# Optimization experiments

Measured on AMD Instinct MI355X. Metric: run time of the kernel, lower is better.

Reference implementation:

```python
import jax, jax.numpy as jnp
import numpy as np
from jax import lax

COCO_80_TO_91 = [1,2,3,4,5,6,7,8,9,10,11,13,14,15,16,17,18,19,20,21,22,23,24,25,27,28,31,32,33,34,35,36,37,38,39,40,41,42,43,44,46,47,48,49,50,51,52,53,54,55,56,57,58,59,60,61,62,63,64,65,67,70,72,73,74,75,76,77,78,79,80,81,82,84,85,86,87,88,89,90]

CONF = 0.25      # self.confidence
IOU_THR = 0.7    # ultralytics NMS default
TOPK = 1000      # candidate cap before NMS
MAX_DET = 300    # ultralytics max_det default
MAX_WH = 7680.0  # per-class offset trick
IMG_SZ = 640.0   # yolov8 letterboxed input size


def setup_inputs() -> dict:
    key = jax.random.key(0)
    preds = jax.random.uniform(key, (32, 84, 8400), dtype=jnp.float32)
    return {"preds": preds}


def _nms_single(boxes, scores):
    """Greedy NMS on score-descending boxes [K,4] (class-offset xyxy). Returns keep mask [K]."""
    K = boxes.shape[0]
    area = (boxes[:, 2] - boxes[:, 0]) * (boxes[:, 3] - boxes[:, 1])  # [K]
    lt = jnp.maximum(boxes[:, None, :2], boxes[None, :, :2])          # [K,K,2]
    rb = jnp.minimum(boxes[:, None, 2:], boxes[None, :, 2:])
    wh = jnp.clip(rb - lt, 0.0)
    inter = wh[..., 0] * wh[..., 1]
    iou = inter / (area[:, None] + area[None, :] - inter + 1e-7)       # [K,K]
    idx = jnp.arange(K)
    sup = (iou > IOU_THR) & (idx[None, :] > idx[:, None])              # i suppresses later j

    def body(i, keep):
        return jnp.where(keep[i], keep & ~sup[i], keep)

    return lax.fori_loop(0, K, body, jnp.ones((K,), dtype=bool))


def reference(preds):
    # preds: [B, 84, N] -> [B, N, 84]
    p = jnp.transpose(preds, (0, 2, 1))
    box_xywh = p[..., :4] * IMG_SZ           # xywh in pixels on 640x640 canvas
    cls = p[..., 4:]                          # [B, N, 80]
    scores = jnp.max(cls, axis=-1)            # best-class confidence
    labels = jnp.argmax(cls, axis=-1)         # 0..79
    xy, wh = box_xywh[..., :2], box_xywh[..., 2:]
    xyxy = jnp.concatenate([xy - wh * 0.5, xy + wh * 0.5], axis=-1)  # decode

    # confidence filter + top-K candidate selection (score-descending)
    s_masked = jnp.where(scores > CONF, scores, -1.0)
    top_s, top_i = lax.top_k(s_masked, TOPK)                          # [B,TOPK]
    top_b = jnp.take_along_axis(xyxy, top_i[..., None], axis=1)      # [B,TOPK,4]
    top_l = jnp.take_along_axis(labels, top_i, axis=1)               # [B,TOPK]

    # per-class NMS via class offset
    off_b = top_b + (top_l.astype(top_b.dtype) * MAX_WH)[..., None]
    keep = jax.vmap(_nms_single)(off_b, top_s) & (top_s > CONF)

    # select final max_det detections, zero-pad invalid slots
    fin_s = jnp.where(keep, top_s, -1.0)
    out_s, out_i = lax.top_k(fin_s, MAX_DET)                          # [B,MAX_DET]
    out_b = jnp.take_along_axis(top_b, out_i[..., None], axis=1)
    out_l = jnp.take_along_axis(top_l, out_i, axis=1)
    valid = out_s > CONF
    boxes = jnp.where(valid[..., None], out_b, 0.0)
    scores_out = jnp.where(valid, out_s, 0.0)
    mapped = jnp.asarray(COCO_80_TO_91, dtype=jnp.int64)[out_l]       # COCO 80 -> 91 ids
    labels_out = jnp.where(valid, mapped, 0)
    return boxes, scores_out, labels_out
```

## Files before the change

kernel.cpp:

```cpp
#include <hip/hip_runtime.h>
#include <stdint.h>

typedef unsigned long long u64;
typedef unsigned int u32;

#define BATCH 32
#define NCH 84
#define NA 8400
#define NCLS 80
#define TOPK 1000
#define MAXDET 300
#define CONF 0.25f
#define IOU_T 0.7f
#define MAX_WH 7680.0f
#define IMG_SZ 640.0f
#define NT 1024
#define KPT 9
#define NCOPY 8
#define HPAD 260
#define DTILE 256

__device__ __constant__ float coco_map_f[NCLS] = {
    1,2,3,4,5,6,7,8,9,10,11,13,14,15,16,17,18,19,20,21,22,23,24,25,27,28,
    31,32,33,34,35,36,37,38,39,40,41,42,43,44,46,47,48,49,50,51,52,53,54,
    55,56,57,58,59,60,61,62,63,64,65,67,70,72,73,74,75,76,77,78,79,80,81,
    82,84,85,86,87,88,89,90};

__device__ inline u64 shflx64(u64 v, int m) {
    int lo = __shfl_xor((int)(u32)(v & 0xFFFFFFFFull), m, 64);
    int hi = __shfl_xor((int)(u32)(v >> 32), m, 64);
    return ((u64)(u32)hi << 32) | (u32)lo;
}

__global__ __launch_bounds__(256)
void decode_kernel(const float* __restrict__ preds,
                   u64* __restrict__ keys,
                   float4* __restrict__ boxes,
                   int* __restrict__ labels) {
    const int b = blockIdx.y;
    const int a_base = blockIdx.x * DTILE;
    const int t = threadIdx.x;
    const int a = a_base + t;
    const float* p = preds + (size_t)b * NCH * NA;

    __shared__ float stage[16][DTILE];

    float bx = 0.f, by = 0.f, bw = 0.f, bh = 0.f;
    float best = -1.0f;
    int bl = 0;

    for (int chunk = 0; chunk < 6; ++chunk) {
        const int r0 = chunk * 16;
        const int nr = (chunk == 5) ? 4 : 16;
        if (chunk) __syncthreads();
        for (int i = 0; i < nr / 4; ++i) {
            int idx = i * 256 + t;
            int rl = idx >> 6;
            int c4 = (idx & 63) * 4;
            int col = a_base + c4;
            float4 v = (col < NA) ? *(const float4*)(p + (size_t)(r0 + rl) * NA + col)
                                  : make_float4(0.f, 0.f, 0.f, 0.f);
            *(float4*)&stage[rl][c4] = v;
        }
        __syncthreads();
        if (chunk == 0) {
            bx = stage[0][t]; by = stage[1][t];
            bw = stage[2][t]; bh = stage[3][t];
            best = stage[4][t]; bl = 0;
            for (int r = 5; r < 16; ++r) {
                float v = stage[r][t];
                int c = r - 4;
                bl = (v > best) ? c : bl;  best = fmaxf(v, best);
            }
        } else {
            for (int r = 0; r < nr; ++r) {
                float v = stage[r][t];
                int c = r0 + r - 4;
                bl = (v > best) ? c : bl;  best = fmaxf(v, best);
            }
        }
    }

    if (a < NA) {
        float fx = bx * IMG_SZ, fy = by * IMG_SZ;
        float fw = bw * IMG_SZ, fh = bh * IMG_SZ;
        float hw = fw * 0.5f, hh = fh * 0.5f;
        boxes[(size_t)b * NA + a] = make_float4(fx - hw, fy - hh, fx + hw, fy + hh);
        float s = (best > CONF) ? best : -1.0f;
        u32 fb = __float_as_uint(s);
        u32 u = (fb & 0x80000000u) ? ~fb : (fb | 0x80000000u);
        keys[(size_t)b * NA + a] = ((u64)u << 14) | (u64)(16383 - a);
        labels[(size_t)b * NA + a] = bl;
    }
}

__global__ __launch_bounds__(NT)
void select_sort_kernel(const u64* __restrict__ keys,
                        const float4* __restrict__ boxes,
                        const int* __restrict__ labels,
                        u64* __restrict__ sortedk,
                        float4* __restrict__ gbox,
                        float4* __restrict__ goffr,
                        float* __restrict__ garear,
                        unsigned char* __restrict__ lbr,
                        float4* __restrict__ goffb,
                        float* __restrict__ garea,
                        unsigned short* __restrict__ grank,
                        int* __restrict__ gccnt) {
    const int b = blockIdx.x;
    const int t = threadIdx.x;
    const int lane = t & 63, wid = t >> 6;

    __shared__ union {
        struct {
            u64 sk[2][NT];
            int hist[NCOPY * HPAD];
        } a;
        struct {
            u64 cmask2[NCLS][16];
        } bb;
    } u_s;
    __shared__ int selB, selK, hselS, smax, scnt, cnt;

    u64 kreg[KPT];
    const u64* kb = keys + (size_t)b * NA;
    int nk = 0;
    for (int i = t; i < NA; i += NT) kreg[nk++] = kb[i];

    u64 P = 0ull;
    int kk = TOPK;
    int nsel = 0;
    for (int d = 5; d >= 0; --d) {
        __syncthreads();
        if (t == 0) { smax = -1; scnt = 0; }
        __syncthreads();
        u64 hmask = (~0ull) << (8 * (d + 1));
        int dig[KPT];
        int mymax = -1;
#pragma unroll
        for (int i = 0; i < KPT; ++i) {
            bool act = (i < nk) && (((kreg[i] ^ P) & hmask) == 0ull);
            dig[i] = act ? (int)((kreg[i] >> (8 * d)) & 255) : -1;
            mymax = max(mymax, dig[i]);
        }
#pragma unroll
        for (int off = 32; off; off >>= 1)
            mymax = max(mymax, __shfl_down(mymax, off, 64));
        if (lane == 0) atomicMax(&smax, mymax);
        __syncthreads();
        int maxb = smax;
        int myc = 0;
#pragma unroll
        for (int i = 0; i < KPT; ++i) myc += (dig[i] == maxb) ? 1 : 0;
#pragma unroll
        for (int off = 32; off; off >>= 1) myc += __shfl_down(myc, off, 64);
        if (lane == 0) atomicAdd(&scnt, myc);
        __syncthreads();
        int cm = scnt;
        if (cm >= kk) {
            P |= ((u64)maxb) << (8 * d);
            nsel = TOPK - kk + cm;
            if (nsel <= NT) break;
            continue;
        }
        for (int i = t; i < NCOPY * HPAD; i += NT) u_s.a.hist[i] = 0;
        __syncthreads();
        int* myh = u_s.a.hist + (wid & (NCOPY - 1)) * HPAD;
#pragma unroll
        for (int i = 0; i < KPT; ++i)
            if (dig[i] >= 0) atomicAdd(&myh[dig[i]], 1);
        __syncthreads();
        if (t < 64) {
            int h0 = 0, h1 = 0, h2 = 0, h3 = 0;
            for (int c = 0; c < NCOPY; ++c) {
                const int* hp = u_s.a.hist + c * HPAD + 4 * t;
                h0 += hp[0]; h1 += hp[1]; h2 += hp[2]; h3 += hp[3];
            }
            int s = h0 + h1 + h2 + h3;
            int S = s;
            #pragma unroll
            for (int off = 1; off < 64; off <<= 1) {
                int o = __shfl_down(S, off, 64);
                if (t + off < 64) S += o;
            }
            int Snext = S - s;
            int c3 = Snext + h3, c2 = c3 + h2, c1 = c2 + h1, c0 = c1 + h0;
            int cand = -1, above = 0;
            if (c0 >= kk) {
                if      (c3 >= kk) { cand = 4 * t + 3; above = Snext; }
                else if (c2 >= kk) { cand = 4 * t + 2; above = c3; }
                else if (c1 >= kk) { cand = 4 * t + 1; above = c2; }
                else               { cand = 4 * t;     above = c1; }
            }
            int pc = (cand < 0) ? 0 : (((cand + 1) << 16) | (kk - above));
            #pragma unroll
            for (int off = 32; off; off >>= 1)
                pc = max(pc, __shfl_down(pc, off, 64));
            pc = __shfl(pc, 0, 64);
            int B = (pc >> 16) - 1;
            if (t == (B >> 2)) {
                int m4 = B & 3;
                selB = B;
                selK = pc & 0xFFFF;
                hselS = (m4 == 0) ? h0 : (m4 == 1) ? h1 : (m4 == 2) ? h2 : h3;
            }
        }
        __syncthreads();
        P |= ((u64)selB) << (8 * d);
        kk = selK;
        nsel = TOPK - kk + hselS;
        if (nsel <= NT) break;
    }

    __syncthreads();
    if (t == 0) cnt = 0;
    __syncthreads();
    for (int i = 0; i < KPT; ++i) {
        bool p = (i < nk) && (kreg[i] >= P);
        u64 m = __ballot(p);
        int base = 0;
        if (lane == 0) base = atomicAdd(&cnt, (int)__popcll(m));
        base = __shfl(base, 0, 64);
        if (p) u_s.a.sk[0][base + (int)__popcll(m & ((1ull << lane) - 1ull))] = kreg[i];
    }
    if (t < NT - nsel) u_s.a.sk[0][nsel + t] = 0ull;
    __syncthreads();

    u64 myk = u_s.a.sk[0][t];
    int buf = 1;
    for (int size = 2; size <= NT; size <<= 1) {
        bool up = ((t & size) == 0);
        for (int stride = size >> 1; stride; stride >>= 1) {
            u64 pk;
            if (stride >= 64) {
                u_s.a.sk[buf][t] = myk;
                __syncthreads();
                pk = u_s.a.sk[buf][t ^ stride];
                buf ^= 1;
            } else {
                pk = shflx64(myk, stride);
            }
            bool tlow = ((t & stride) == 0);
            u64 mn = (myk < pk) ? myk : pk;
            u64 mx = (myk < pk) ? pk : myk;
            myk = up ? (tlow ? mx : mn) : (tlow ? mn : mx);
        }
    }
    sortedk[(size_t)b * NT + t] = myk;

    __syncthreads();
    for (int i = t; i < NCLS * 16; i += NT) ((u64*)u_s.bb.cmask2)[i] = 0ull;
    __syncthreads();

    int my_L = 0;
    float4 bx = make_float4(0.f, 0.f, 0.f, 0.f);
    float ox0 = 0.f, oy0 = 0.f, ox1 = 0.f, oy1 = 0.f, ar = 0.f;
    if (t < TOPK) {
        int my_a = 16383 - (int)(myk & 16383ull);
        my_L = labels[(size_t)b * NA + my_a];
        bx = boxes[(size_t)b * NA + my_a];
        float off = (float)my_L * MAX_WH;
        ox0 = bx.x + off; oy0 = bx.y + off; ox1 = bx.z + off; oy1 = bx.w + off;
        ar = (ox1 - ox0) * (oy1 - oy0);
        atomicOr(&u_s.bb.cmask2[my_L][t >> 6], 1ull << (t & 63));
    }
    __syncthreads();
    if (t < TOPK) {
        int w = t >> 6;
        int r = __popcll(u_s.bb.cmask2[my_L][w] & ((1ull << (t & 63)) - 1ull));
        for (int q = 0; q < w; ++q) r += __popcll(u_s.bb.cmask2[my_L][q]);
        gbox[(size_t)b * NT + t] = bx;
        goffr[(size_t)b * NT + t] = make_float4(ox0, oy0, ox1, oy1);
        garear[(size_t)b * NT + t] = ar;
        lbr[(size_t)b * NT + t] = (unsigned char)my_L;
        if (r < 64) {
            size_t ci = ((size_t)b * NCLS + my_L) * 64 + r;
            goffb[ci] = make_float4(ox0, oy0, ox1, oy1);
            garea[ci] = ar;
            grank[ci] = (unsigned short)t;
        }
    }
    if (t < NCLS) {
        int s = 0;
#pragma unroll
        for (int q = 0; q < 16; ++q) s += __popcll(u_s.bb.cmask2[t][q]);
        gccnt[(size_t)b * NCLS + t] = s;
    }
}

__global__ __launch_bounds__(64)
void nms_kernel(const float4* __restrict__ goffb,
                const float* __restrict__ garea,
                const unsigned short* __restrict__ grank,
                const int* __restrict__ gccnt,
                const float4* __restrict__ goffr,
                const float* __restrict__ garear,
                const unsigned char* __restrict__ lbr,
                unsigned char* __restrict__ keepg) {
    const int c = blockIdx.x;
    const int b = blockIdx.y;
    const int lane = threadIdx.x;
    const int n = gccnt[(size_t)b * NCLS + c];
    if (n == 0) return;

    if (n <= 64) {
        size_t ci = ((size_t)b * NCLS + c) * 64 + lane;
        float4 bb = make_float4(0.f, 0.f, 0.f, 0.f);
        float ar = 0.f;
        int rk = 0;
        if (lane < n) { bb = goffb[ci]; ar = garea[ci]; rk = grank[ci]; }
        u64 colm = 0ull;
        for (int i = 0; i < n; ++i) {
            float hx0 = __shfl(bb.x, i, 64);
            float hy0 = __shfl(bb.y, i, 64);
            float hx1 = __shfl(bb.z, i, 64);
            float hy1 = __shfl(bb.w, i, 64);
            float ha  = __shfl(ar, i, 64);
            float lx = fmaxf(hx0, bb.x), ly = fmaxf(hy0, bb.y);
            float rx = fminf(hx1, bb.z), ry = fminf(hy1, bb.w);
            float w = fmaxf(rx - lx, 0.0f);
            float h = fmaxf(ry - ly, 0.0f);
            float inter = w * h;
            float denom = ha + ar;
            denom = denom - inter;
            denom = denom + 1e-7f;
            bool s = (lane > i) && (lane < n) && (inter / denom > IOU_T);
            colm |= ((u64)s) << i;
        }
        u64 alive = (n >= 64) ? ~0ull : ((1ull << n) - 1ull);
        for (int i = 0; i < n; ++i) {
            if (!((alive >> i) & 1ull)) continue;
            alive &= ~__ballot((colm >> i) & 1ull);
        }
        if (lane < n) keepg[(size_t)b * NT + rk] = (unsigned char)((alive >> lane) & 1ull);
    } else if (lane == 0) {
        u64 aliveW[16];
        for (int q = 0; q < 16; ++q) aliveW[q] = ~0ull;
        for (int i = 0; i < TOPK; ++i) {
            if (lbr[(size_t)b * NT + i] != (unsigned char)c) continue;
            if (!((aliveW[i >> 6] >> (i & 63)) & 1ull)) continue;
            float4 bi = goffr[(size_t)b * NT + i];
            float ai = garear[(size_t)b * NT + i];
            for (int j = i + 1; j < TOPK; ++j) {
                if (lbr[(size_t)b * NT + j] != (unsigned char)c) continue;
                if (!((aliveW[j >> 6] >> (j & 63)) & 1ull)) continue;
                float4 bj = goffr[(size_t)b * NT + j];
                float lx = fmaxf(bi.x, bj.x), ly = fmaxf(bi.y, bj.y);
                float rx = fminf(bi.z, bj.z), ry = fminf(bi.w, bj.w);
                float w = fmaxf(rx - lx, 0.0f);
                float h = fmaxf(ry - ly, 0.0f);
                float inter = w * h;
                float denom = ai + garear[(size_t)b * NT + j];
                denom = denom - inter;
                denom = denom + 1e-7f;
                if (inter / denom > IOU_T) aliveW[j >> 6] &= ~(1ull << (j & 63));
            }
        }
        for (int i = 0; i < TOPK; ++i)
            if (lbr[(size_t)b * NT + i] == (unsigned char)c)
                keepg[(size_t)b * NT + i] = (unsigned char)((aliveW[i >> 6] >> (i & 63)) & 1ull);
    }
}

__global__ __launch_bounds__(NT)
void epilogue_kernel(const u64* __restrict__ sortedk,
                     const unsigned char* __restrict__ keepg,
                     const float4* __restrict__ gbox,
                     const unsigned char* __restrict__ lbr,
                     float* __restrict__ out) {
    const int b = blockIdx.x;
    const int t = threadIdx.x;
    const int lane = t & 63, wid = t >> 6;
    __shared__ int wsum[16], woff[16], ktot_s;

    u64 myk = sortedk[(size_t)b * NT + t];
    bool valid = false;
    float sj = 0.0f;
    if (t < TOPK) {
        u32 u = (u32)(myk >> 14);
        u32 fb = (u & 0x80000000u) ? (u ^ 0x80000000u) : ~u;
        sj = __uint_as_float(fb);
        valid = keepg[(size_t)b * NT + t] && (sj > CONF);
    }
    u64 m = __ballot(valid);
    if (lane == 0) wsum[wid] = (int)__popcll(m);
    __syncthreads();
    if (wid == 0) {
        int v = (lane < 16) ? wsum[lane] : 0;
        #pragma unroll
        for (int off = 1; off < 16; off <<= 1) {
            int o = __shfl_up(v, off, 64);
            if (lane >= off) v += o;
        }
        if (lane < 16) woff[lane] = v - wsum[lane];
        if (lane == 15) ktot_s = v;
    }
    __syncthreads();
    int ktot = ktot_s;
    int rank = woff[wid] + (int)__popcll(m & ((1ull << lane) - 1ull));

    float* out_boxes = out;
    float* out_scores = out + (size_t)BATCH * MAXDET * 4;
    float* out_labels = out + (size_t)BATCH * MAXDET * 5;
    if (valid && rank < MAXDET) {
        float4 bx = gbox[(size_t)b * NT + t];
        float* ob = out_boxes + ((size_t)b * MAXDET + rank) * 4;
        ob[0] = bx.x; ob[1] = bx.y; ob[2] = bx.z; ob[3] = bx.w;
        out_scores[(size_t)b * MAXDET + rank] = sj;
        out_labels[(size_t)b * MAXDET + rank] = coco_map_f[lbr[(size_t)b * NT + t]];
    }
    if (t < MAXDET && t >= ktot) {
        float* ob = out_boxes + ((size_t)b * MAXDET + t) * 4;
        ob[0] = 0.0f; ob[1] = 0.0f; ob[2] = 0.0f; ob[3] = 0.0f;
        out_scores[(size_t)b * MAXDET + t] = 0.0f;
        out_labels[(size_t)b * MAXDET + t] = 0.0f;
    }
}

extern "C" void kernel_launch(void* const* d_in, const int* in_sizes, int n_in,
                              void* d_out, int out_size, void* d_ws, size_t ws_size,
                              hipStream_t stream) {
    const float* preds = (const float*)d_in[0];
    char* ws = (char*)d_ws;
    size_t off = 0;
    auto alloc = [&](size_t bytes) { char* p = ws + off; off += (bytes + 255) & ~(size_t)255; return p; };

    u64* keys            = (u64*)           alloc((size_t)BATCH * NA * 8);
    float4* boxes        = (float4*)        alloc((size_t)BATCH * NA * 16);
    int* labels          = (int*)           alloc((size_t)BATCH * NA * 4);
    u64* sortedk         = (u64*)           alloc((size_t)BATCH * NT * 8);
    float4* gbox         = (float4*)        alloc((size_t)BATCH * NT * 16);
    float4* goffr        = (float4*)        alloc((size_t)BATCH * NT * 16);
    float* garear        = (float*)         alloc((size_t)BATCH * NT * 4);
    unsigned char* lbr   = (unsigned char*) alloc((size_t)BATCH * NT);
    float4* goffb        = (float4*)        alloc((size_t)BATCH * NCLS * 64 * 16);
    float* garea         = (float*)         alloc((size_t)BATCH * NCLS * 64 * 4);
    unsigned short* grank= (unsigned short*)alloc((size_t)BATCH * NCLS * 64 * 2);
    int* gccnt           = (int*)           alloc((size_t)BATCH * NCLS * 4);
    unsigned char* keepg = (unsigned char*) alloc((size_t)BATCH * NT);
    float* out = (float*)d_out;

    dim3 dgrid((NA + DTILE - 1) / DTILE, BATCH);
    decode_kernel<<<dgrid, 256, 0, stream>>>(preds, keys, boxes, labels);
    select_sort_kernel<<<BATCH, NT, 0, stream>>>(keys, boxes, labels, sortedk,
                                                 gbox, goffr, garear, lbr,
                                                 goffb, garea, grank, gccnt);
    dim3 ngrid(NCLS, BATCH);
    nms_kernel<<<ngrid, 64, 0, stream>>>(goffb, garea, grank, gccnt,
                                         goffr, garear, lbr, keepg);
    epilogue_kernel<<<BATCH, NT, 0, stream>>>(sortedk, keepg, gbox, lbr, out);
}
```

Baseline: 172.5 us.

## Fuse select, NMS and epilogue into one kernel; pack labels into sort keys

```diff
diff --git a/kernel.cpp b/kernel.cpp
--- a/kernel.cpp
+++ b/kernel.cpp
@@ -35,8 +35,7 @@
 __global__ __launch_bounds__(256)
 void decode_kernel(const float* __restrict__ preds,
                    u64* __restrict__ keys,
-                   float4* __restrict__ boxes,
-                   int* __restrict__ labels) {
+                   float4* __restrict__ boxes) {
     const int b = blockIdx.y;
     const int a_base = blockIdx.x * DTILE;
     const int t = threadIdx.x;
@@ -89,24 +88,15 @@
         float s = (best > CONF) ? best : -1.0f;
         u32 fb = __float_as_uint(s);
         u32 u = (fb & 0x80000000u) ? ~fb : (fb | 0x80000000u);
-        keys[(size_t)b * NA + a] = ((u64)u << 14) | (u64)(16383 - a);
-        labels[(size_t)b * NA + a] = bl;
+        keys[(size_t)b * NA + a] =
+            ((u64)u << 21) | ((u64)(16383 - a) << 7) | (u64)bl;
     }
 }
 
 __global__ __launch_bounds__(NT)
-void select_sort_kernel(const u64* __restrict__ keys,
-                        const float4* __restrict__ boxes,
-                        const int* __restrict__ labels,
-                        u64* __restrict__ sortedk,
-                        float4* __restrict__ gbox,
-                        float4* __restrict__ goffr,
-                        float* __restrict__ garear,
-                        unsigned char* __restrict__ lbr,
-                        float4* __restrict__ goffb,
-                        float* __restrict__ garea,
-                        unsigned short* __restrict__ grank,
-                        int* __restrict__ gccnt) {
+void fused_kernel(const u64* __restrict__ keys,
+                  const float4* __restrict__ boxes,
+                  float* __restrict__ out) {
     const int b = blockIdx.x;
     const int t = threadIdx.x;
     const int lane = t & 63, wid = t >> 6;
@@ -119,8 +109,17 @@
         struct {
             u64 cmask2[NCLS][16];
         } bb;
+        struct {
+            float4 obox[NT];
+            float  area[NT];
+            unsigned short ranks[NCLS][64];
+            int    cnt[NCLS];
+            unsigned char cls[NT];
+            unsigned char keep[NT];
+        } c;
     } u_s;
-    __shared__ int selB, selK, hselS, smax, scnt, cnt;
+    __shared__ int selB, selK, hselS, smax, scnt, cnt_s;
+    __shared__ int wsum[16], woff[16], ktot_s;
 
     u64 kreg[KPT];
     const u64* kb = keys + (size_t)b * NA;
@@ -130,7 +129,7 @@
     u64 P = 0ull;
     int kk = TOPK;
     int nsel = 0;
-    for (int d = 5; d >= 0; --d) {
+    for (int d = 6; d >= 0; --d) {
         __syncthreads();
         if (t == 0) { smax = -1; scnt = 0; }
         __syncthreads();
@@ -213,13 +212,13 @@
     }
 
     __syncthreads();
-    if (t == 0) cnt = 0;
+    if (t == 0) cnt_s = 0;
     __syncthreads();
     for (int i = 0; i < KPT; ++i) {
         bool p = (i < nk) && (kreg[i] >= P);
         u64 m = __ballot(p);
         int base = 0;
-        if (lane == 0) base = atomicAdd(&cnt, (int)__popcll(m));
+        if (lane == 0) base = atomicAdd(&cnt_s, (int)__popcll(m));
         base = __shfl(base, 0, 64);
         if (p) u_s.a.sk[0][base + (int)__popcll(m & ((1ull << lane) - 1ull))] = kreg[i];
     }
@@ -246,151 +245,127 @@
             myk = up ? (tlow ? mx : mn) : (tlow ? mn : mx);
         }
     }
-    sortedk[(size_t)b * NT + t] = myk;
 
     __syncthreads();
     for (int i = t; i < NCLS * 16; i += NT) ((u64*)u_s.bb.cmask2)[i] = 0ull;
     __syncthreads();
 
     int my_L = 0;
+    float sj = -1.0f;
     float4 bx = make_float4(0.f, 0.f, 0.f, 0.f);
-    float ox0 = 0.f, oy0 = 0.f, ox1 = 0.f, oy1 = 0.f, ar = 0.f;
     if (t < TOPK) {
-        int my_a = 16383 - (int)(myk & 16383ull);
-        my_L = labels[(size_t)b * NA + my_a];
+        int my_a = 16383 - (int)((myk >> 7) & 16383ull);
+        my_L = (int)(myk & 127ull);
         bx = boxes[(size_t)b * NA + my_a];
-        float off = (float)my_L * MAX_WH;
-        ox0 = bx.x + off; oy0 = bx.y + off; ox1 = bx.z + off; oy1 = bx.w + off;
-        ar = (ox1 - ox0) * (oy1 - oy0);
+        u32 u = (u32)(myk >> 21);
+        u32 fb = (u & 0x80000000u) ? (u ^ 0x80000000u) : ~u;
+        sj = __uint_as_float(fb);
         atomicOr(&u_s.bb.cmask2[my_L][t >> 6], 1ull << (t & 63));
     }
     __syncthreads();
+    int r = 0, cntreg = 0;
     if (t < TOPK) {
         int w = t >> 6;
-        int r = __popcll(u_s.bb.cmask2[my_L][w] & ((1ull << (t & 63)) - 1ull));
+        r = __popcll(u_s.bb.cmask2[my_L][w] & ((1ull << (t & 63)) - 1ull));
         for (int q = 0; q < w; ++q) r += __popcll(u_s.bb.cmask2[my_L][q]);
-        gbox[(size_t)b * NT + t] = bx;
-        goffr[(size_t)b * NT + t] = make_float4(ox0, oy0, ox1, oy1);
-        garear[(size_t)b * NT + t] = ar;
-        lbr[(size_t)b * NT + t] = (unsigned char)my_L;
-        if (r < 64) {
-            size_t ci = ((size_t)b * NCLS + my_L) * 64 + r;
-            goffb[ci] = make_float4(ox0, oy0, ox1, oy1);
-            garea[ci] = ar;
-            grank[ci] = (unsigned short)t;
-        }
     }
     if (t < NCLS) {
-        int s = 0;
-#pragma unroll
-        for (int q = 0; q < 16; ++q) s += __popcll(u_s.bb.cmask2[t][q]);
-        gccnt[(size_t)b * NCLS + t] = s;
-    }
-}
-
-__global__ __launch_bounds__(64)
-void nms_kernel(const float4* __restrict__ goffb,
-                const float* __restrict__ garea,
-                const unsigned short* __restrict__ grank,
-                const int* __restrict__ gccnt,
-                const float4* __restrict__ goffr,
-                const float* __restrict__ garear,
-                const unsigned char* __restrict__ lbr,
-                unsigned char* __restrict__ keepg) {
-    const int c = blockIdx.x;
-    const int b = blockIdx.y;
-    const int lane = threadIdx.x;
-    const int n = gccnt[(size_t)b * NCLS + c];
-    if (n == 0) return;
-
-    if (n <= 64) {
-        size_t ci = ((size_t)b * NCLS + c) * 64 + lane;
-        float4 bb = make_float4(0.f, 0.f, 0.f, 0.f);
-        float ar = 0.f;
-        int rk = 0;
-        if (lane < n) { bb = goffb[ci]; ar = garea[ci]; rk = grank[ci]; }
-        u64 colm = 0ull;
-        for (int i = 0; i < n; ++i) {
-            float hx0 = __shfl(bb.x, i, 64);
-            float hy0 = __shfl(bb.y, i, 64);
-            float hx1 = __shfl(bb.z, i, 64);
-            float hy1 = __shfl(bb.w, i, 64);
-            float ha  = __shfl(ar, i, 64);
-            float lx = fmaxf(hx0, bb.x), ly = fmaxf(hy0, bb.y);
-            float rx = fminf(hx1, bb.z), ry = fminf(hy1, bb.w);
-            float w = fmaxf(rx - lx, 0.0f);
-            float h = fmaxf(ry - ly, 0.0f);
-            float inter = w * h;
-            float denom = ha + ar;
-            denom = denom - inter;
-            denom = denom + 1e-7f;
-            bool s = (lane > i) && (lane < n) && (inter / denom > IOU_T);
-            colm |= ((u64)s) << i;
-        }
-        u64 alive = (n >= 64) ? ~0ull : ((1ull << n) - 1ull);
-        for (int i = 0; i < n; ++i) {
-            if (!((alive >> i) & 1ull)) continue;
-            alive &= ~__ballot((colm >> i) & 1ull);
-        }
-        if (lane < n) keepg[(size_t)b * NT + rk] = (unsigned char)((alive >> lane) & 1ull);
-    } else if (lane == 0) {
-        u64 aliveW[16];
-        for (int q = 0; q < 16; ++q) aliveW[q] = ~0ull;
-        for (int i = 0; i < TOPK; ++i) {
-            if (lbr[(size_t)b * NT + i] != (unsigned char)c) continue;
-            if (!((aliveW[i >> 6] >> (i & 63)) & 1ull)) continue;
-            float4 bi = goffr[(size_t)b * NT + i];
-            float ai = garear[(size_t)b * NT + i];
-            for (int j = i + 1; j < TOPK; ++j) {
-                if (lbr[(size_t)b * NT + j] != (unsigned char)c) continue;
-                if (!((aliveW[j >> 6] >> (j & 63)) & 1ull)) continue;
-                float4 bj = goffr[(size_t)b * NT + j];
-                float lx = fmaxf(bi.x, bj.x), ly = fmaxf(bi.y, bj.y);
-                float rx = fminf(bi.z, bj.z), ry = fminf(bi.w, bj.w);
+#pragma unroll
+        for (int q = 0; q < 16; ++q) cntreg += __popcll(u_s.bb.cmask2[t][q]);
+    }
+    __syncthreads();
+
+    float off = (float)my_L * MAX_WH;
+    float ox0 = bx.x + off, oy0 = bx.y + off, ox1 = bx.z + off, oy1 = bx.w + off;
+    float ar = (ox1 - ox0) * (oy1 - oy0);
+    if (t < TOPK) {
+        u_s.c.obox[t] = make_float4(ox0, oy0, ox1, oy1);
+        u_s.c.area[t] = ar;
+        u_s.c.cls[t]  = (unsigned char)my_L;
+        if (r < 64) u_s.c.ranks[my_L][r] = (unsigned short)t;
+    } else {
+        u_s.c.cls[t] = 255;
+    }
+    u_s.c.keep[t] = 0;
+    if (t < NCLS) u_s.c.cnt[t] = cntreg;
+    __syncthreads();
+
+    for (int cc = wid; cc < NCLS; cc += 16) {
+        int n = u_s.c.cnt[cc];
+        if (n == 0) continue;
+        if (n <= 64) {
+            float4 bbx = make_float4(0.f, 0.f, 0.f, 0.f);
+            float aa = 0.f;
+            int rk = 0;
+            if (lane < n) {
+                rk  = u_s.c.ranks[cc][lane];
+                bbx = u_s.c.obox[rk];
+                aa  = u_s.c.area[rk];
+            }
+            u64 colm = 0ull;
+            for (int i = 0; i < n; ++i) {
+                float hx0 = __shfl(bbx.x, i, 64);
+                float hy0 = __shfl(bbx.y, i, 64);
+                float hx1 = __shfl(bbx.z, i, 64);
+                float hy1 = __shfl(bbx.w, i, 64);
+                float ha  = __shfl(aa, i, 64);
+                float lx = fmaxf(hx0, bbx.x), ly = fmaxf(hy0, bbx.y);
+                float rx = fminf(hx1, bbx.z), ry = fminf(hy1, bbx.w);
                 float w = fmaxf(rx - lx, 0.0f);
                 float h = fmaxf(ry - ly, 0.0f);
                 float inter = w * h;
-                float denom = ai + garear[(size_t)b * NT + j];
+                float denom = ha + aa;
                 denom = denom - inter;
                 denom = denom + 1e-7f;
-                if (inter / denom > IOU_T) aliveW[j >> 6] &= ~(1ull << (j & 63));
-            }
-        }
-        for (int i = 0; i < TOPK; ++i)
-            if (lbr[(size_t)b * NT + i] == (unsigned char)c)
-                keepg[(size_t)b * NT + i] = (unsigned char)((aliveW[i >> 6] >> (i & 63)) & 1ull);
-    }
-}
-
-__global__ __launch_bounds__(NT)
-void epilogue_kernel(const u64* __restrict__ sortedk,
-                     const unsigned char* __restrict__ keepg,
-                     const float4* __restrict__ gbox,
-                     const unsigned char* __restrict__ lbr,
-                     float* __restrict__ out) {
-    const int b = blockIdx.x;
-    const int t = threadIdx.x;
-    const int lane = t & 63, wid = t >> 6;
-    __shared__ int wsum[16], woff[16], ktot_s;
-
-    u64 myk = sortedk[(size_t)b * NT + t];
-    bool valid = false;
-    float sj = 0.0f;
-    if (t < TOPK) {
-        u32 u = (u32)(myk >> 14);
-        u32 fb = (u & 0x80000000u) ? (u ^ 0x80000000u) : ~u;
-        sj = __uint_as_float(fb);
-        valid = keepg[(size_t)b * NT + t] && (sj > CONF);
-    }
+                bool s = (lane > i) && (lane < n) && (inter / denom > IOU_T);
+                colm |= ((u64)s) << i;
+            }
+            u64 alive = (n >= 64) ? ~0ull : ((1ull << n) - 1ull);
+            for (int i = 0; i < n; ++i) {
+                if (!((alive >> i) & 1ull)) continue;
+                alive &= ~__ballot((colm >> i) & 1ull);
+            }
+            if (lane < n) u_s.c.keep[rk] = (unsigned char)((alive >> lane) & 1ull);
+        } else if (lane == 0) {
+            u64 aliveW[16];
+            for (int q = 0; q < 16; ++q) aliveW[q] = ~0ull;
+            for (int i = 0; i < TOPK; ++i) {
+                if (u_s.c.cls[i] != (unsigned char)cc) continue;
+                if (!((aliveW[i >> 6] >> (i & 63)) & 1ull)) continue;
+                float4 bi = u_s.c.obox[i];
+                float ai = u_s.c.area[i];
+                for (int j = i + 1; j < TOPK; ++j) {
+                    if (u_s.c.cls[j] != (unsigned char)cc) continue;
+                    if (!((aliveW[j >> 6] >> (j & 63)) & 1ull)) continue;
+                    float4 bj = u_s.c.obox[j];
+                    float lx = fmaxf(bi.x, bj.x), ly = fmaxf(bi.y, bj.y);
+                    float rx = fminf(bi.z, bj.z), ry = fminf(bi.w, bj.w);
+                    float w = fmaxf(rx - lx, 0.0f);
+                    float h = fmaxf(ry - ly, 0.0f);
+                    float inter = w * h;
+                    float denom = ai + u_s.c.area[j];
+                    denom = denom - inter;
+                    denom = denom + 1e-7f;
+                    if (inter / denom > IOU_T) aliveW[j >> 6] &= ~(1ull << (j & 63));
+                }
+            }
+            for (int i = 0; i < TOPK; ++i)
+                if (u_s.c.cls[i] == (unsigned char)cc)
+                    u_s.c.keep[i] = (unsigned char)((aliveW[i >> 6] >> (i & 63)) & 1ull);
+        }
+    }
+    __syncthreads();
+
+    bool valid = (t < TOPK) && u_s.c.keep[t] && (sj > CONF);
     u64 m = __ballot(valid);
     if (lane == 0) wsum[wid] = (int)__popcll(m);
     __syncthreads();
     if (wid == 0) {
         int v = (lane < 16) ? wsum[lane] : 0;
         #pragma unroll
-        for (int off = 1; off < 16; off <<= 1) {
-            int o = __shfl_up(v, off, 64);
-            if (lane >= off) v += o;
+        for (int o = 1; o < 16; o <<= 1) {
+            int x = __shfl_up(v, o, 64);
+            if (lane >= o) v += x;
         }
         if (lane < 16) woff[lane] = v - wsum[lane];
         if (lane == 15) ktot_s = v;
@@ -403,11 +378,10 @@
     float* out_scores = out + (size_t)BATCH * MAXDET * 4;
     float* out_labels = out + (size_t)BATCH * MAXDET * 5;
     if (valid && rank < MAXDET) {
-        float4 bx = gbox[(size_t)b * NT + t];
         float* ob = out_boxes + ((size_t)b * MAXDET + rank) * 4;
         ob[0] = bx.x; ob[1] = bx.y; ob[2] = bx.z; ob[3] = bx.w;
         out_scores[(size_t)b * MAXDET + rank] = sj;
-        out_labels[(size_t)b * MAXDET + rank] = coco_map_f[lbr[(size_t)b * NT + t]];
+        out_labels[(size_t)b * MAXDET + rank] = coco_map_f[my_L];
     }
     if (t < MAXDET && t >= ktot) {
         float* ob = out_boxes + ((size_t)b * MAXDET + t) * 4;
@@ -425,28 +399,11 @@
     size_t off = 0;
     auto alloc = [&](size_t bytes) { char* p = ws + off; off += (bytes + 255) & ~(size_t)255; return p; };
 
-    u64* keys            = (u64*)           alloc((size_t)BATCH * NA * 8);
-    float4* boxes        = (float4*)        alloc((size_t)BATCH * NA * 16);
-    int* labels          = (int*)           alloc((size_t)BATCH * NA * 4);
-    u64* sortedk         = (u64*)           alloc((size_t)BATCH * NT * 8);
-    float4* gbox         = (float4*)        alloc((size_t)BATCH * NT * 16);
-    float4* goffr        = (float4*)        alloc((size_t)BATCH * NT * 16);
-    float* garear        = (float*)         alloc((size_t)BATCH * NT * 4);
-    unsigned char* lbr   = (unsigned char*) alloc((size_t)BATCH * NT);
-    float4* goffb        = (float4*)        alloc((size_t)BATCH * NCLS * 64 * 16);
-    float* garea         = (float*)         alloc((size_t)BATCH * NCLS * 64 * 4);
-    unsigned short* grank= (unsigned short*)alloc((size_t)BATCH * NCLS * 64 * 2);
-    int* gccnt           = (int*)           alloc((size_t)BATCH * NCLS * 4);
-    unsigned char* keepg = (unsigned char*) alloc((size_t)BATCH * NT);
+    u64* keys     = (u64*)    alloc((size_t)BATCH * NA * 8);
+    float4* boxes = (float4*) alloc((size_t)BATCH * NA * 16);
     float* out = (float*)d_out;
 
     dim3 dgrid((NA + DTILE - 1) / DTILE, BATCH);
-    decode_kernel<<<dgrid, 256, 0, stream>>>(preds, keys, boxes, labels);
-    select_sort_kernel<<<BATCH, NT, 0, stream>>>(keys, boxes, labels, sortedk,
-                                                 gbox, goffr, garear, lbr,
-                                                 goffb, garea, grank, gccnt);
-    dim3 ngrid(NCLS, BATCH);
-    nms_kernel<<<ngrid, 64, 0, stream>>>(goffb, garea, grank, gccnt,
-                                         goffr, garear, lbr, keepg);
-    epilogue_kernel<<<BATCH, NT, 0, stream>>>(sortedk, keepg, gbox, lbr, out);
+    decode_kernel<<<dgrid, 256, 0, stream>>>(preds, keys, boxes);
+    fused_kernel<<<BATCH, NT, 0, stream>>>(keys, boxes, out);
 }
```

Measured after the change: 189.4 us. +9.8%, slower.
